# Performance work log

Measured on AMD Instinct MI355X. Metric: run time of the kernel, lower is better.

The kernel has to match this reference:

```python
import jax, jax.numpy as jnp
import numpy as np

N_NODES = 50000
N_EDGES = 800000
N_GRAPHS = 256
F_IN, HID, EMB = 128, 256, 128
N_GROUPS, N_FAM = 16, 128


def setup_inputs() -> dict:
    key = jax.random.key(0)
    ks = jax.random.split(key, 12)
    x = jax.random.normal(ks[0], (N_NODES, F_IN), dtype=jnp.float32)
    edge_index = jax.random.randint(ks[1], (2, N_EDGES), 0, N_NODES, dtype=jnp.int64)
    batch = jnp.sort(jax.random.randint(ks[2], (N_NODES,), 0, N_GRAPHS, dtype=jnp.int64))
    def lin(k, fi, fo):
        s = 1.0 / np.sqrt(fi)
        return jax.random.uniform(k, (fi, fo), minval=-s, maxval=s, dtype=jnp.float32)
    W1 = lin(ks[3], F_IN, HID); b1 = jnp.zeros((HID,), jnp.float32)
    W2 = lin(ks[4], HID, EMB); b2 = jnp.zeros((EMB,), jnp.float32)
    Wg = lin(ks[5], EMB, N_GROUPS); bg = jnp.zeros((N_GROUPS,), jnp.float32)
    s = 1.0 / np.sqrt(EMB)
    Wf = jax.random.uniform(ks[6], (N_GROUPS, EMB, N_FAM), minval=-s, maxval=s, dtype=jnp.float32)
    bf = jnp.zeros((N_GROUPS, N_FAM), jnp.float32)
    return {"x": x, "edge_index": edge_index, "batch": batch,
            "W1": W1, "b1": b1, "W2": W2, "b2": b2,
            "Wg": Wg, "bg": bg, "Wf": Wf, "bf": bf}


def _gcn_conv(h, src, dst, coef, W, b, n):
    # h: [N, Fin]; src/dst: [E'] (self-loops included); coef: [E'] sym-norm
    hw = h @ W                                    # [N, Fout]
    msg = hw[src] * coef[:, None]                 # gather + scale, [E', Fout]
    out = jax.ops.segment_sum(msg, dst, num_segments=n)  # scatter-add
    return out + b


def reference(x, edge_index, batch, W1, b1, W2, b2, Wg, bg, Wf, bf):
    n = x.shape[0]
    loops = jnp.arange(n, dtype=edge_index.dtype)
    src = jnp.concatenate([edge_index[0], loops])
    dst = jnp.concatenate([edge_index[1], loops])
    # symmetric GCN normalization (deg >= 1 thanks to self-loops)
    deg = jax.ops.segment_sum(jnp.ones_like(dst, dtype=x.dtype), dst, num_segments=n)
    dinv = jax.lax.rsqrt(deg)
    coef = dinv[src] * dinv[dst]

    h1 = jax.nn.relu(_gcn_conv(x, src, dst, coef, W1, b1, n))  # dropout = identity (eval)
    h2 = _gcn_conv(h1, src, dst, coef, W2, b2, n)

    # global mean pool over graphs
    sums = jax.ops.segment_sum(h2, batch, num_segments=N_GRAPHS)
    cnts = jax.ops.segment_sum(jnp.ones((n,), x.dtype), batch, num_segments=N_GRAPHS)
    embeddings = sums / jnp.maximum(cnts, 1.0)[:, None]        # [G, EMB]

    group_logits = embeddings @ Wg + bg                        # [G, n_groups]
    pred_groups = jnp.argmax(group_logits, axis=1)             # routing
    # per-graph routed family classifier (dense equivalent of the dict outputs)
    family_logits = jnp.einsum('gd,gdf->gf', embeddings, Wf[pred_groups]) + bf[pred_groups]
    return embeddings, group_logits, family_logits
```

## Files before the change

kernel.cpp:

```cpp
#include <hip/hip_runtime.h>
#include <hip/hip_fp16.h>
#include <cstddef>
#include <cstdint>

static constexpr int NN   = 50000;
static constexpr int NE   = 800000;
static constexpr int NG   = 256;
static constexpr int FIN  = 128;
static constexpr int HID  = 256;
static constexpr int EMB  = 128;
static constexpr int NGRP = 16;
static constexpr int NFAM = 128;
static constexpr int NETOT = NE + NN;

static constexpr int SCAN_B  = 256;
static constexpr int SCAN_CH = (NN + SCAN_B - 1) / SCAN_B;

using bf16x8 = __attribute__((ext_vector_type(8))) short;
using f32x4  = __attribute__((ext_vector_type(4))) float;

__device__ __forceinline__ unsigned short f2bf(float f) {
    uint32_t u = __float_as_uint(f);
    u += 0x7FFFu + ((u >> 16) & 1u);
    return (unsigned short)(u >> 16);
}
__device__ __forceinline__ float bf2f(unsigned short u) {
    return __uint_as_float((uint32_t)u << 16);
}
__device__ __forceinline__ uint32_t pack_sw(int s, float w) {
    return (uint32_t)s | ((uint32_t)__half_as_ushort(__float2half(w)) << 16);
}
__device__ __forceinline__ void unpack_sw(uint32_t v, int& s, float& w) {
    s = (int)(v & 0xFFFFu);
    w = __half2float(__ushort_as_half((unsigned short)(v >> 16)));
}


__global__ void k_init_deg(int* __restrict__ degi, int n) {
    int i = blockIdx.x * blockDim.x + threadIdx.x;
    if (i < n) degi[i] = 1;
}

__global__ void k_count(const int* __restrict__ edst, int* __restrict__ degi, int e) {
    int i = blockIdx.x * blockDim.x + threadIdx.x;
    if (i < e) atomicAdd(degi + edst[i], 1);
}

__global__ void k_prep(const int* __restrict__ degi, const int* __restrict__ batch,
                       float* __restrict__ dinv, int* __restrict__ gstart,
                       float* __restrict__ emb_acc, int n, int G) {
    int i = blockIdx.x * blockDim.x + threadIdx.x;
    if (i < NG * EMB) emb_acc[i] = 0.f;
    if (i >= n) return;
    dinv[i] = rsqrtf((float)degi[i]);
    int b  = batch[i];
    int pb = (i == 0) ? -1 : batch[i - 1];
    for (int g = pb + 1; g <= b; ++g) gstart[g] = i;
    if (i == n - 1) {
        for (int g = b + 1; g <= G; ++g) gstart[g] = n;
    }
}

__global__ void k_xconv(const float* __restrict__ x, const float* __restrict__ dinv,
                        unsigned short* __restrict__ xs) {
    int t = blockIdx.x * blockDim.x + threadIdx.x;
    size_t i = (size_t)t * 8;
    float dv = dinv[t >> 4];
    float4 a = *(const float4*)(x + i);
    float4 b = *(const float4*)(x + i + 4);
    uint4 o;
    o.x = (uint32_t)f2bf(dv * a.x) | ((uint32_t)f2bf(dv * a.y) << 16);
    o.y = (uint32_t)f2bf(dv * a.z) | ((uint32_t)f2bf(dv * a.w) << 16);
    o.z = (uint32_t)f2bf(dv * b.x) | ((uint32_t)f2bf(dv * b.y) << 16);
    o.w = (uint32_t)f2bf(dv * b.z) | ((uint32_t)f2bf(dv * b.w) << 16);
    *(uint4*)(xs + i) = o;
}

__global__ void k_w1t(const float* __restrict__ W1, unsigned short* __restrict__ W1t) {
    int t = blockIdx.x * blockDim.x + threadIdx.x;
    int nidx = t >> 7, k = t & 127;
    W1t[t] = f2bf(W1[(size_t)k * HID + nidx]);
}

__global__ void k_w2t(const float* __restrict__ W2, unsigned short* __restrict__ W2t) {
    int t = blockIdx.x * blockDim.x + threadIdx.x;
    int nidx = t >> 8, k = t & 255;
    W2t[t] = f2bf(W2[(size_t)k * EMB + nidx]);
}


__global__ __launch_bounds__(256) void k_scanA(const int* __restrict__ degi,
                                               int* __restrict__ row_ptr,
                                               int* __restrict__ bsum, int n) {
    __shared__ int sh[256];
    const int b = blockIdx.x, t = threadIdx.x;
    const int idx = b * SCAN_CH + t;
    int v = 0;
    if (t < SCAN_CH && idx < n) v = degi[idx];
    sh[t] = v;
    __syncthreads();
    for (int off = 1; off < 256; off <<= 1) {
        int y = (t >= off) ? sh[t - off] : 0;
        __syncthreads();
        if (t >= off) sh[t] += y;
        __syncthreads();
    }
    if (t < SCAN_CH && idx < n) row_ptr[idx] = sh[t] - v;
    if (t == 255) bsum[b] = sh[255];
}

__global__ __launch_bounds__(256) void k_scanB(const int* __restrict__ bsum,
                                               const int* __restrict__ gstart,
                                               float* __restrict__ rcnt,
                                               int* __restrict__ row_ptr,
                                               int* __restrict__ cursor, int n) {
    __shared__ int sh[SCAN_B];
    const int b = blockIdx.x, t = threadIdx.x;
    sh[t] = bsum[t];
    __syncthreads();
    for (int off = 1; off < SCAN_B; off <<= 1) {
        int y = (t >= off) ? sh[t - off] : 0;
        __syncthreads();
        if (t >= off) sh[t] += y;
        __syncthreads();
    }
    const int boff = (b == 0) ? 0 : sh[b - 1];
    const int idx  = b * SCAN_CH + t;
    if (t < SCAN_CH && idx < n) {
        row_ptr[idx] += boff;
        cursor[idx] = 1;
    }
    if (b == 0 && t == 0) row_ptr[n] = sh[SCAN_B - 1];
    if (b == 0 && t < NG) {
        int c = gstart[t + 1] - gstart[t];
        rcnt[t] = 1.0f / (float)max(c, 1);
    }
}

__global__ void k_build(const int* __restrict__ esrc, const int* __restrict__ edst,
                        const int* __restrict__ batch, const float* __restrict__ dinv,
                        const float* __restrict__ rcnt, const int* __restrict__ row_ptr,
                        int* __restrict__ cursor, int* __restrict__ eA,
                        uint32_t* __restrict__ eP, int n, int e) {
    int i = blockIdx.x * blockDim.x + threadIdx.x;
    if (i < n) {
        int p = row_ptr[i];
        eA[p] = i;
        eP[p] = pack_sw(i, dinv[i] * rcnt[batch[i]]);
    } else if (i < n + e) {
        int ei = i - n;
        int d = edst[ei], s = esrc[ei];
        int p = atomicAdd(cursor + d, 1);
        int idx = row_ptr[d] + p;
        eA[idx] = s;
        eP[idx] = pack_sw(s, dinv[d] * rcnt[batch[d]]);
    }
}


__global__ __launch_bounds__(256) void k_agg(
        const unsigned short* __restrict__ xs, const int* __restrict__ row_ptr,
        const int* __restrict__ eA, const float* __restrict__ dinv,
        unsigned short* __restrict__ xa, int n) {
    int node = blockIdx.x * 4 + (threadIdx.x >> 6);
    if (node >= n) return;
    int lane = threadIdx.x & 63;
    int grp = lane >> 4, fl = lane & 15;
    float acc[8] = {};
    int beg = row_ptr[node], end = row_ptr[node + 1];
    for (int j = beg; j < end; j += 4) {
        int jj = j + grp;
        bool valid = jj < end;
        int s = __builtin_nontemporal_load(eA + (valid ? jj : beg));
        float m = valid ? 1.f : 0.f;
        bf16x8 v = *(const bf16x8*)(xs + ((size_t)s << 7) + fl * 8);
#pragma unroll
        for (int k = 0; k < 8; ++k)
            acc[k] += m * bf2f((unsigned short)v[k]);
    }
#pragma unroll
    for (int k = 0; k < 8; ++k) {
        acc[k] += __shfl_xor(acc[k], 16);
        acc[k] += __shfl_xor(acc[k], 32);
    }
    if (lane < 16) {
        float di = dinv[node];
        uint4 o;
        o.x = (uint32_t)f2bf(di * acc[0]) | ((uint32_t)f2bf(di * acc[1]) << 16);
        o.y = (uint32_t)f2bf(di * acc[2]) | ((uint32_t)f2bf(di * acc[3]) << 16);
        o.z = (uint32_t)f2bf(di * acc[4]) | ((uint32_t)f2bf(di * acc[5]) << 16);
        o.w = (uint32_t)f2bf(di * acc[6]) | ((uint32_t)f2bf(di * acc[7]) << 16);
        *(uint4*)(xa + ((size_t)node << 7) + fl * 8) = o;
    }
}


__global__ __launch_bounds__(256) void k_fgemm(
        const unsigned short* __restrict__ A,
        const unsigned short* __restrict__ W1t,
        const unsigned short* __restrict__ W2t,
        const float* __restrict__ b1, const float* __restrict__ dinv,
        unsigned short* __restrict__ H, int M) {
    __shared__ unsigned short h1s[64 * 256];
    const int m0 = blockIdx.x * 64;
    const int w  = threadIdx.x >> 6;
    const int l  = threadIdx.x & 63;
    const int lr = l & 15;
    const int lk = l >> 4;

    {
        f32x4 acc[4][4] = {};
        const int n0 = w * 64;
#pragma unroll
        for (int ks = 0; ks < 4; ++ks) {
            const int k0 = ks * 32 + lk * 8;
            bf16x8 bfr[4];
#pragma unroll
            for (int ni = 0; ni < 4; ++ni)
                bfr[ni] = *(const bf16x8*)(W1t + (size_t)(n0 + ni * 16 + lr) * FIN + k0);
#pragma unroll
            for (int mi = 0; mi < 4; ++mi) {
                int row = min(m0 + mi * 16 + lr, M - 1);
                bf16x8 afr = *(const bf16x8*)(A + ((size_t)row << 7) + k0);
#pragma unroll
                for (int ni = 0; ni < 4; ++ni)
                    acc[mi][ni] = __builtin_amdgcn_mfma_f32_16x16x32_bf16(
                        afr, bfr[ni], acc[mi][ni], 0, 0, 0);
            }
        }
#pragma unroll
        for (int ni = 0; ni < 4; ++ni) {
            int col = n0 + ni * 16 + lr;
            float bb = b1[col];
#pragma unroll
            for (int mi = 0; mi < 4; ++mi) {
#pragma unroll
                for (int r = 0; r < 4; ++r) {
                    int rl = mi * 16 + lk * 4 + r;
                    float dv = dinv[min(m0 + rl, M - 1)];
                    float v = fmaxf(acc[mi][ni][r] + bb, 0.f) * dv;
                    int byte = (rl * 512 + col * 2) ^ ((rl & 7) << 4);
                    *(unsigned short*)((char*)h1s + byte) = f2bf(v);
                }
            }
        }
    }
    __syncthreads();
    f32x4 acc2[4][2] = {};
    {
        const int n0 = w * 32;
#pragma unroll
        for (int ks = 0; ks < 8; ++ks) {
            const int k0 = ks * 32 + lk * 8;
            bf16x8 bfr[2];
#pragma unroll
            for (int ni = 0; ni < 2; ++ni)
                bfr[ni] = *(const bf16x8*)(W2t + (size_t)(n0 + ni * 16 + lr) * HID + k0);
#pragma unroll
            for (int mi = 0; mi < 4; ++mi) {
                int rl = mi * 16 + lr;
                int byte = (rl * 512 + k0 * 2) ^ ((rl & 7) << 4);
                bf16x8 afr = *(const bf16x8*)((const char*)h1s + byte);
#pragma unroll
                for (int ni = 0; ni < 2; ++ni)
                    acc2[mi][ni] = __builtin_amdgcn_mfma_f32_16x16x32_bf16(
                        afr, bfr[ni], acc2[mi][ni], 0, 0, 0);
            }
        }
    }
    __syncthreads();
    {
        const int n0 = w * 32;
#pragma unroll
        for (int ni = 0; ni < 2; ++ni) {
            int col = n0 + ni * 16 + lr;
#pragma unroll
            for (int mi = 0; mi < 4; ++mi)
#pragma unroll
                for (int r = 0; r < 4; ++r) {
                    int rl = mi * 16 + lk * 4 + r;
                    h1s[rl * EMB + col] = f2bf(acc2[mi][ni][r]);
                }
        }
    }
    __syncthreads();
    int nrows = min(64, M - m0);
    for (int c = threadIdx.x; c < nrows * 16; c += 256) {
        int rl = c >> 4, cc = c & 15;
        *(uint4*)(H + ((size_t)(m0 + rl) << 7) + cc * 8) =
            *(const uint4*)(h1s + rl * EMB + cc * 8);
    }
}


__global__ __launch_bounds__(256) void k_pool(
        const unsigned short* __restrict__ H, const int* __restrict__ row_ptr,
        const int* __restrict__ gstart, const uint32_t* __restrict__ eP,
        float* __restrict__ emb_acc) {
    __shared__ float red[4][EMB];
    const int g  = blockIdx.x >> 3;
    const int kb = blockIdx.x & 7;
    const int e0 = row_ptr[gstart[g]];
    const int e1 = row_ptr[gstart[g + 1]];
    const int len = e1 - e0;
    const int per = (len + 7) >> 3;
    const int s0  = e0 + kb * per;
    const int s1  = min(s0 + per, e1);
    const int lane = threadIdx.x & 63;
    const int wv   = threadIdx.x >> 6;
    const int grp = lane >> 4, fl = lane & 15;

    float acc[8] = {};
    for (int j = s0 + wv * 4; j < s1; j += 16) {
        int jj = j + grp;
        bool valid = jj < s1;
        uint32_t ev = __builtin_nontemporal_load(eP + (valid ? jj : s0));
        int s; float wgt;
        unpack_sw(ev, s, wgt);
        if (!valid) wgt = 0.f;
        bf16x8 v = *(const bf16x8*)(H + ((size_t)s << 7) + fl * 8);
#pragma unroll
        for (int k = 0; k < 8; ++k)
            acc[k] += wgt * bf2f((unsigned short)v[k]);
    }
#pragma unroll
    for (int k = 0; k < 8; ++k) {
        acc[k] += __shfl_xor(acc[k], 16);
        acc[k] += __shfl_xor(acc[k], 32);
    }
    if (lane < 16) {
#pragma unroll
        for (int k = 0; k < 8; ++k) red[wv][fl * 8 + k] = acc[k];
    }
    __syncthreads();
    int t = threadIdx.x;
    if (t < EMB) {
        float v = red[0][t] + red[1][t] + red[2][t] + red[3][t];
        if (v != 0.f) atomicAdd(&emb_acc[g * EMB + t], v);
    }
}


__global__ __launch_bounds__(128) void k_head(const float* __restrict__ emb_acc,
                                              const int* __restrict__ gstart,
                                              const float* __restrict__ b2,
                                              const float* __restrict__ Wg,
                                              const float* __restrict__ bg,
                                              const float* __restrict__ Wf,
                                              const float* __restrict__ bff,
                                              float* __restrict__ out_emb,
                                              float* __restrict__ out_gl,
                                              float* __restrict__ out_fl) {
    __shared__ float e[EMB];
    __shared__ float gl[NGRP];
    __shared__ int ps;
    int g = blockIdx.x, c = threadIdx.x;
    bool nonempty = gstart[g + 1] > gstart[g];
    float a = emb_acc[g * EMB + c] + (nonempty ? b2[c] : 0.f);
    e[c] = a;
    out_emb[(size_t)g * EMB + c] = a;
    __syncthreads();
    if (c < NGRP) {
        float s = bg[c];
        for (int d = 0; d < EMB; ++d) s += e[d] * Wg[d * NGRP + c];
        gl[c] = s;
        out_gl[g * NGRP + c] = s;
    }
    __syncthreads();
    if (c == 0) {
        int bi = 0;
        float bv = gl[0];
        for (int t2 = 1; t2 < NGRP; ++t2)
            if (gl[t2] > bv) { bv = gl[t2]; bi = t2; }
        ps = bi;
    }
    __syncthreads();
    int pr = ps;
    float s = bff[pr * NFAM + c];
    for (int d = 0; d < EMB; ++d) s += e[d] * Wf[((size_t)pr * EMB + d) * NFAM + c];
    out_fl[g * NFAM + c] = s;
}


extern "C" void kernel_launch(void* const* d_in, const int* in_sizes, int n_in,
                              void* d_out, int out_size, void* d_ws, size_t ws_size,
                              hipStream_t stream) {
    const float* x   = (const float*)d_in[0];
    const int*   ei  = (const int*)d_in[1];
    const int*   bat = (const int*)d_in[2];
    const float* W1  = (const float*)d_in[3];
    const float* b1  = (const float*)d_in[4];
    const float* W2  = (const float*)d_in[5];
    const float* b2  = (const float*)d_in[6];
    const float* Wg  = (const float*)d_in[7];
    const float* bg  = (const float*)d_in[8];
    const float* Wf  = (const float*)d_in[9];
    const float* bf  = (const float*)d_in[10];

    float* out     = (float*)d_out;
    float* out_emb = out;
    float* out_gl  = out + (size_t)NG * EMB;
    float* out_fl  = out_gl + (size_t)NG * NGRP;

    char* w = (char*)d_ws;
    auto alloc = [&](size_t bytes) {
        char* p = w;
        w += (bytes + 255) & ~(size_t)255;
        return p;
    };
    int*            degi    = (int*)alloc((size_t)NN * 4);
    float*          dinv    = (float*)alloc((size_t)NN * 4);
    int*            row_ptr = (int*)alloc((size_t)(NN + 1) * 4);
    int*            cursor  = (int*)alloc((size_t)NN * 4);
    int*            bsum    = (int*)alloc((size_t)SCAN_B * 4);
    int*            eA      = (int*)alloc((size_t)NETOT * 4);
    uint32_t*       eP      = (uint32_t*)alloc((size_t)NETOT * 4);
    int*            gstart  = (int*)alloc((size_t)(NG + 1) * 4);
    float*          rcnt    = (float*)alloc((size_t)NG * 4);
    unsigned short* xs      = (unsigned short*)alloc((size_t)NN * FIN * 2);
    unsigned short* xa      = (unsigned short*)alloc((size_t)NN * FIN * 2);
    unsigned short* W1t     = (unsigned short*)alloc((size_t)HID * FIN * 2);
    unsigned short* W2t     = (unsigned short*)alloc((size_t)EMB * HID * 2);
    unsigned short* H       = (unsigned short*)alloc((size_t)NN * EMB * 2);
    float*          emb_acc = (float*)alloc((size_t)NG * EMB * 4);

    const int* esrc = ei;
    const int* edst = ei + NE;

    k_init_deg<<<(NN + 255) / 256, 256, 0, stream>>>(degi, NN);
    k_count<<<(NE + 255) / 256, 256, 0, stream>>>(edst, degi, NE);
    k_prep<<<(NG * HID + 255) / 256, 256, 0, stream>>>(degi, bat, dinv, gstart,
                                                       emb_acc, NN, NG);
    k_xconv<<<(NN * 16) / 256, 256, 0, stream>>>(x, dinv, xs);
    k_w1t<<<(HID * FIN) / 256, 256, 0, stream>>>(W1, W1t);
    k_w2t<<<(EMB * HID) / 256, 256, 0, stream>>>(W2, W2t);
    k_scanA<<<SCAN_B, 256, 0, stream>>>(degi, row_ptr, bsum, NN);
    k_scanB<<<SCAN_B, 256, 0, stream>>>(bsum, gstart, rcnt, row_ptr, cursor, NN);
    k_build<<<(NETOT + 255) / 256, 256, 0, stream>>>(esrc, edst, bat, dinv, rcnt,
                                                     row_ptr, cursor, eA, eP, NN, NE);

    k_agg<<<(NN + 3) / 4, 256, 0, stream>>>(xs, row_ptr, eA, dinv, xa, NN);
    k_fgemm<<<(NN + 63) / 64, 256, 0, stream>>>(xa, W1t, W2t, b1, dinv, H, NN);

    k_pool<<<NG * 8, 256, 0, stream>>>(H, row_ptr, gstart, eP, emb_acc);

    k_head<<<NG, 128, 0, stream>>>(emb_acc, gstart, b2, Wg, bg, Wf, bf,
                                   out_emb, out_gl, out_fl);
}
```

Measured before the change: 216.6 us.

## Slice CSR build by destination range and drop separate source-index array

Rewrites the CSR build so each block handles one of eight destination-node slices. Every block scans all edges but only scatters edges whose destination falls in its slice, which aims to localise atomics and scattered writes into an L2-sized region. The separate eA array is removed and aggregation decodes the source index from the packed eP word, cutting one write and one read stream. Kernel launches are also merged: deg init becomes a memset with +1 applied at use, and the two weight-conversion kernels become one. In exchange every edge is read eight times across slices.

```diff
diff --git a/kernel.cpp b/kernel.cpp
--- a/kernel.cpp
+++ b/kernel.cpp
@@ -16,6 +16,10 @@
 static constexpr int SCAN_B  = 256;
 static constexpr int SCAN_CH = (NN + SCAN_B - 1) / SCAN_B;
 
+static constexpr int NSLICE  = 8;
+static constexpr int SLICE_W = (NN + NSLICE - 1) / NSLICE;
+static constexpr int BUILD_RANKS = 64;
+
 using bf16x8 = __attribute__((ext_vector_type(8))) short;
 using f32x4  = __attribute__((ext_vector_type(4))) float;
 
@@ -35,11 +39,6 @@
     w = __half2float(__ushort_as_half((unsigned short)(v >> 16)));
 }
 
-
-__global__ void k_init_deg(int* __restrict__ degi, int n) {
-    int i = blockIdx.x * blockDim.x + threadIdx.x;
-    if (i < n) degi[i] = 1;
-}
 
 __global__ void k_count(const int* __restrict__ edst, int* __restrict__ degi, int e) {
     int i = blockIdx.x * blockDim.x + threadIdx.x;
@@ -52,7 +51,7 @@
     int i = blockIdx.x * blockDim.x + threadIdx.x;
     if (i < NG * EMB) emb_acc[i] = 0.f;
     if (i >= n) return;
-    dinv[i] = rsqrtf((float)degi[i]);
+    dinv[i] = rsqrtf((float)(degi[i] + 1));
     int b  = batch[i];
     int pb = (i == 0) ? -1 : batch[i - 1];
     for (int g = pb + 1; g <= b; ++g) gstart[g] = i;
@@ -76,16 +75,17 @@
     *(uint4*)(xs + i) = o;
 }
 
-__global__ void k_w1t(const float* __restrict__ W1, unsigned short* __restrict__ W1t) {
+__global__ void k_wconv(const float* __restrict__ W1, const float* __restrict__ W2,
+                        unsigned short* __restrict__ W1t, unsigned short* __restrict__ W2t) {
     int t = blockIdx.x * blockDim.x + threadIdx.x;
-    int nidx = t >> 7, k = t & 127;
-    W1t[t] = f2bf(W1[(size_t)k * HID + nidx]);
-}
-
-__global__ void k_w2t(const float* __restrict__ W2, unsigned short* __restrict__ W2t) {
-    int t = blockIdx.x * blockDim.x + threadIdx.x;
-    int nidx = t >> 8, k = t & 255;
-    W2t[t] = f2bf(W2[(size_t)k * EMB + nidx]);
+    if (t < HID * FIN) {
+        int nidx = t >> 7, k = t & 127;
+        W1t[t] = f2bf(W1[(size_t)k * HID + nidx]);
+    } else {
+        int u = t - HID * FIN;
+        int nidx = u >> 8, k = u & 255;
+        W2t[u] = f2bf(W2[(size_t)k * EMB + nidx]);
+    }
 }
 
 
@@ -96,7 +96,7 @@
     const int b = blockIdx.x, t = threadIdx.x;
     const int idx = b * SCAN_CH + t;
     int v = 0;
-    if (t < SCAN_CH && idx < n) v = degi[idx];
+    if (t < SCAN_CH && idx < n) v = degi[idx] + 1;
     sh[t] = v;
     __syncthreads();
     for (int off = 1; off < 256; off <<= 1) {
@@ -137,30 +137,32 @@
     }
 }
 
-__global__ void k_build(const int* __restrict__ esrc, const int* __restrict__ edst,
-                        const int* __restrict__ batch, const float* __restrict__ dinv,
-                        const float* __restrict__ rcnt, const int* __restrict__ row_ptr,
-                        int* __restrict__ cursor, int* __restrict__ eA,
-                        uint32_t* __restrict__ eP, int n, int e) {
-    int i = blockIdx.x * blockDim.x + threadIdx.x;
-    if (i < n) {
-        int p = row_ptr[i];
-        eA[p] = i;
-        eP[p] = pack_sw(i, dinv[i] * rcnt[batch[i]]);
-    } else if (i < n + e) {
-        int ei = i - n;
-        int d = edst[ei], s = esrc[ei];
+
+__global__ __launch_bounds__(256) void k_build(
+        const int* __restrict__ esrc, const int* __restrict__ edst,
+        const int* __restrict__ batch, const float* __restrict__ dinv,
+        const float* __restrict__ rcnt, const int* __restrict__ row_ptr,
+        int* __restrict__ cursor, uint32_t* __restrict__ eP, int n, int e) {
+    const int slice = blockIdx.x & 7;
+    const int rank  = blockIdx.x >> 3;
+    const int lo = slice * SLICE_W;
+    const int hi = min(lo + SLICE_W, n);
+    for (int i = lo + rank * 256 + (int)threadIdx.x; i < hi; i += BUILD_RANKS * 256) {
+        eP[row_ptr[i]] = pack_sw(i, dinv[i] * rcnt[batch[i]]);
+    }
+    for (int j = rank * 256 + (int)threadIdx.x; j < e; j += BUILD_RANKS * 256) {
+        int d = edst[j];
+        if (d < lo || d >= hi) continue;
+        int s = esrc[j];
         int p = atomicAdd(cursor + d, 1);
-        int idx = row_ptr[d] + p;
-        eA[idx] = s;
-        eP[idx] = pack_sw(s, dinv[d] * rcnt[batch[d]]);
+        eP[row_ptr[d] + p] = pack_sw(s, dinv[d] * rcnt[batch[d]]);
     }
 }
 
 
 __global__ __launch_bounds__(256) void k_agg(
         const unsigned short* __restrict__ xs, const int* __restrict__ row_ptr,
-        const int* __restrict__ eA, const float* __restrict__ dinv,
+        const uint32_t* __restrict__ eP, const float* __restrict__ dinv,
         unsigned short* __restrict__ xa, int n) {
     int node = blockIdx.x * 4 + (threadIdx.x >> 6);
     if (node >= n) return;
@@ -171,7 +173,8 @@
     for (int j = beg; j < end; j += 4) {
         int jj = j + grp;
         bool valid = jj < end;
-        int s = __builtin_nontemporal_load(eA + (valid ? jj : beg));
+        uint32_t ev = __builtin_nontemporal_load(eP + (valid ? jj : beg));
+        int s = (int)(ev & 0xFFFFu);
         float m = valid ? 1.f : 0.f;
         bf16x8 v = *(const bf16x8*)(xs + ((size_t)s << 7) + fl * 8);
 #pragma unroll
@@ -413,7 +416,6 @@
     int*            row_ptr = (int*)alloc((size_t)(NN + 1) * 4);
     int*            cursor  = (int*)alloc((size_t)NN * 4);
     int*            bsum    = (int*)alloc((size_t)SCAN_B * 4);
-    int*            eA      = (int*)alloc((size_t)NETOT * 4);
     uint32_t*       eP      = (uint32_t*)alloc((size_t)NETOT * 4);
     int*            gstart  = (int*)alloc((size_t)(NG + 1) * 4);
     float*          rcnt    = (float*)alloc((size_t)NG * 4);
@@ -427,19 +429,18 @@
     const int* esrc = ei;
     const int* edst = ei + NE;
 
-    k_init_deg<<<(NN + 255) / 256, 256, 0, stream>>>(degi, NN);
+    hipMemsetAsync(degi, 0, (size_t)NN * 4, stream);
     k_count<<<(NE + 255) / 256, 256, 0, stream>>>(edst, degi, NE);
     k_prep<<<(NG * HID + 255) / 256, 256, 0, stream>>>(degi, bat, dinv, gstart,
                                                        emb_acc, NN, NG);
     k_xconv<<<(NN * 16) / 256, 256, 0, stream>>>(x, dinv, xs);
-    k_w1t<<<(HID * FIN) / 256, 256, 0, stream>>>(W1, W1t);
-    k_w2t<<<(EMB * HID) / 256, 256, 0, stream>>>(W2, W2t);
+    k_wconv<<<(HID * FIN + EMB * HID) / 256, 256, 0, stream>>>(W1, W2, W1t, W2t);
     k_scanA<<<SCAN_B, 256, 0, stream>>>(degi, row_ptr, bsum, NN);
     k_scanB<<<SCAN_B, 256, 0, stream>>>(bsum, gstart, rcnt, row_ptr, cursor, NN);
-    k_build<<<(NETOT + 255) / 256, 256, 0, stream>>>(esrc, edst, bat, dinv, rcnt,
-                                                     row_ptr, cursor, eA, eP, NN, NE);
-
-    k_agg<<<(NN + 3) / 4, 256, 0, stream>>>(xs, row_ptr, eA, dinv, xa, NN);
+    k_build<<<NSLICE * BUILD_RANKS, 256, 0, stream>>>(esrc, edst, bat, dinv, rcnt,
+                                                      row_ptr, cursor, eP, NN, NE);
+
+    k_agg<<<(NN + 3) / 4, 256, 0, stream>>>(xs, row_ptr, eP, dinv, xa, NN);
     k_fgemm<<<(NN + 63) / 64, 256, 0, stream>>>(xa, W1t, W2t, b1, dinv, H, NN);
 
     k_pool<<<NG * 8, 256, 0, stream>>>(H, row_ptr, gstart, eP, emb_acc);
```

After: 223.4 us. 3.1% more time.
